# Kernel optimization log

Measured on AMD Instinct MI355X. Metric: run time of the kernel, lower is better.

Reference implementation:

```python
import jax, jax.numpy as jnp
import numpy as np

ENCODER_DIM, DECODER_DIM, ATTN_DIM = 2048, 512, 512
B, P = 128, 196  # batch, num_pixels (14x14)


def setup_inputs() -> dict:
    key = jax.random.key(0)
    ks = jax.random.split(key, 8)
    s_e = 1.0 / np.sqrt(ENCODER_DIM)
    s_d = 1.0 / np.sqrt(DECODER_DIM)
    s_a = 1.0 / np.sqrt(ATTN_DIM)
    return {
        "encoder_out": jax.random.normal(ks[0], (B, P, ENCODER_DIM), jnp.float32),
        "decoder_hidden": jax.random.normal(ks[1], (B, DECODER_DIM), jnp.float32),
        "W_enc": jax.random.uniform(ks[2], (ENCODER_DIM, ATTN_DIM), jnp.float32, -s_e, s_e),
        "b_enc": jax.random.uniform(ks[3], (ATTN_DIM,), jnp.float32, -s_e, s_e),
        "W_dec": jax.random.uniform(ks[4], (DECODER_DIM, ATTN_DIM), jnp.float32, -s_d, s_d),
        "b_dec": jax.random.uniform(ks[5], (ATTN_DIM,), jnp.float32, -s_d, s_d),
        "W_full": jax.random.uniform(ks[6], (ATTN_DIM,), jnp.float32, -s_a, s_a),
        "b_full": jax.random.uniform(ks[7], (), jnp.float32, -s_a, s_a),
    }


def reference(encoder_out, decoder_hidden, W_enc, b_enc, W_dec, b_dec, W_full, b_full):
    # att1: [B, P, A]; att2: [B, A]
    att1 = jnp.einsum("bpe,ea->bpa", encoder_out, W_enc) + b_enc
    att2 = decoder_hidden @ W_dec + b_dec
    # broadcast add + relu + score projection -> [B, P]
    att = jax.nn.relu(att1 + att2[:, None, :]) @ W_full + b_full
    alpha = jax.nn.softmax(att, axis=1)  # over pixels
    # weighted sum over pixels -> [B, E]
    attention_weighted_encoding = jnp.einsum("bpe,bp->be", encoder_out, alpha)
    return (attention_weighted_encoding, alpha)
```

## Files before the change

kernel.cpp:

```cpp
#include <hip/hip_runtime.h>
#include <hip/hip_bf16.h>

#define ENC_DIM 2048
#define DEC_DIM 512
#define ATT_DIM 512
#define BATCH   128
#define NPIX    196
#define NROWS   (BATCH * NPIX)

typedef short bf16x8 __attribute__((ext_vector_type(8)));
typedef float f32x4  __attribute__((ext_vector_type(4)));
typedef unsigned short u16x8 __attribute__((ext_vector_type(8)));

__device__ __forceinline__ unsigned short f2bf(float f) {
    union { float f; unsigned u; } v; v.f = f;
    unsigned r = v.u + 0x7fffu + ((v.u >> 16) & 1u);
    return (unsigned short)(r >> 16);
}

__global__ void k0_transpose(const float* __restrict__ W_enc,
                             unsigned short* __restrict__ Wt) {
    __shared__ float ts[64][65];
    const int a0 = blockIdx.x * 64;
    const int e0 = blockIdx.y * 64;
    const int tx = threadIdx.x & 15;
    const int ty = threadIdx.x >> 4;
    #pragma unroll
    for (int p = 0; p < 4; ++p) {
        const int e = ty + p * 16;
        const float4 v = *(const float4*)&W_enc[(size_t)(e0 + e) * ATT_DIM + a0 + tx * 4];
        ts[e][tx * 4 + 0] = v.x; ts[e][tx * 4 + 1] = v.y;
        ts[e][tx * 4 + 2] = v.z; ts[e][tx * 4 + 3] = v.w;
    }
    __syncthreads();
    #pragma unroll
    for (int p = 0; p < 4; ++p) {
        const int a = ty + p * 16;
        ushort4 u;
        u.x = f2bf(ts[tx * 4 + 0][a]);
        u.y = f2bf(ts[tx * 4 + 1][a]);
        u.z = f2bf(ts[tx * 4 + 2][a]);
        u.w = f2bf(ts[tx * 4 + 3][a]);
        *(ushort4*)&Wt[(size_t)(a0 + a) * ENC_DIM + e0 + tx * 4] = u;
    }
}

__global__ void k1_att2(const float* __restrict__ dh, const float* __restrict__ W_dec,
                        const float* __restrict__ b_dec, const float* __restrict__ b_enc,
                        const float* __restrict__ b_full,
                        float* __restrict__ att2, float* __restrict__ att) {
    __shared__ float dhs[DEC_DIM];
    const int b = blockIdx.x, t = threadIdx.x;
    dhs[t]       = dh[b * DEC_DIM + t];
    dhs[t + 256] = dh[b * DEC_DIM + t + 256];
    __syncthreads();
    float acc0 = 0.f, acc1 = 0.f;
    for (int d = 0; d < DEC_DIM; ++d) {
        const float h = dhs[d];
        acc0 += h * W_dec[d * ATT_DIM + t];
        acc1 += h * W_dec[d * ATT_DIM + t + 256];
    }
    att2[b * ATT_DIM + t]       = acc0 + b_dec[t]       + b_enc[t];
    att2[b * ATT_DIM + t + 256] = acc1 + b_dec[t + 256] + b_enc[t + 256];
    const int gid = b * 256 + t;
    if (gid < NROWS) att[gid] = b_full[0];
}

__launch_bounds__(256, 4)
__global__ void k2_gemm(const float* __restrict__ enc, const unsigned short* __restrict__ Wt,
                        const float* __restrict__ att2, const float* __restrict__ W_full,
                        float* __restrict__ att) {
    __shared__ __align__(16) unsigned short As[64 * 72];
    __shared__ __align__(16) unsigned short Bs[128 * 72];
    __shared__ float att2s[2][128];
    __shared__ float wfs[128];

    const int t    = threadIdx.x;
    const int n0   = blockIdx.x * 128;
    const int row0 = blockIdx.y * 64;
    const int b0   = row0 / NPIX;
    const int rows_left = (b0 + 1) * NPIX - row0;

    if (t < 128) {
        att2s[0][t] = att2[b0 * ATT_DIM + n0 + t];
        att2s[1][t] = (b0 + 1 < BATCH) ? att2[(b0 + 1) * ATT_DIM + n0 + t] : 0.f;
        wfs[t]      = W_full[n0 + t];
    }

    const int w    = t >> 6;
    const int lane = t & 63;
    const int q    = lane >> 4;
    const int cl   = lane & 15;
    const int wm   = (w >> 1) * 32;
    const int wn   = (w & 1) * 64;

    f32x4 acc[2][4] = {};

    const int ar = t >> 3;
    const int ak = (t & 7) * 8;
    const int bn = t >> 2;
    const int bk = (t & 3) * 16;

    const float*          encA = enc + (size_t)(row0 + ar) * ENC_DIM + ak;
    const unsigned short* WtB  = Wt  + (size_t)(n0 + bn)   * ENC_DIM + bk;

    for (int k0 = 0; k0 < ENC_DIM; k0 += 64) {
        __syncthreads();
        #pragma unroll
        for (int p = 0; p < 2; ++p) {
            const float4 v0 = *(const float4*)(encA + (size_t)p * 32 * ENC_DIM + k0);
            const float4 v1 = *(const float4*)(encA + (size_t)p * 32 * ENC_DIM + k0 + 4);
            u16x8 u;
            u[0] = f2bf(v0.x); u[1] = f2bf(v0.y); u[2] = f2bf(v0.z); u[3] = f2bf(v0.w);
            u[4] = f2bf(v1.x); u[5] = f2bf(v1.y); u[6] = f2bf(v1.z); u[7] = f2bf(v1.w);
            *(u16x8*)&As[(ar + p * 32) * 72 + ak] = u;
        }
        #pragma unroll
        for (int p = 0; p < 2; ++p) {
            const uint4 v0 = *(const uint4*)(WtB + (size_t)p * 64 * ENC_DIM + k0);
            const uint4 v1 = *(const uint4*)(WtB + (size_t)p * 64 * ENC_DIM + k0 + 8);
            *(uint4*)&Bs[(bn + p * 64) * 72 + bk]     = v0;
            *(uint4*)&Bs[(bn + p * 64) * 72 + bk + 8] = v1;
        }
        __syncthreads();

        #pragma unroll
        for (int h = 0; h < 2; ++h) {
            bf16x8 af[2], bfr[4];
            #pragma unroll
            for (int i = 0; i < 2; ++i)
                af[i]  = *(const bf16x8*)&As[(wm + i * 16 + cl) * 72 + h * 32 + q * 8];
            #pragma unroll
            for (int i = 0; i < 4; ++i)
                bfr[i] = *(const bf16x8*)&Bs[(wn + i * 16 + cl) * 72 + h * 32 + q * 8];
            #pragma unroll
            for (int mi = 0; mi < 2; ++mi)
                #pragma unroll
                for (int ni = 0; ni < 4; ++ni)
                    acc[mi][ni] = __builtin_amdgcn_mfma_f32_16x16x32_bf16(
                        af[mi], bfr[ni], acc[mi][ni], 0, 0, 0);
        }
    }

    #pragma unroll
    for (int mi = 0; mi < 2; ++mi) {
        float rs[4];
        #pragma unroll
        for (int i = 0; i < 4; ++i) {
            const int lr  = wm + mi * 16 + q * 4 + i;
            const int sel = (lr >= rows_left) ? 1 : 0;
            float sum = 0.f;
            #pragma unroll
            for (int ni = 0; ni < 4; ++ni) {
                const int j = wn + ni * 16 + cl;
                float v = acc[mi][ni][i] + att2s[sel][j];
                v = fmaxf(v, 0.f);
                sum += v * wfs[j];
            }
            rs[i] = sum;
        }
        #pragma unroll
        for (int o = 1; o < 16; o <<= 1) {
            #pragma unroll
            for (int i = 0; i < 4; ++i) rs[i] += __shfl_xor(rs[i], o);
        }
        if (cl == 0) {
            #pragma unroll
            for (int i = 0; i < 4; ++i) {
                const int r = row0 + wm + mi * 16 + q * 4 + i;
                atomicAdd(&att[r], rs[i]);
            }
        }
    }
}

__global__ void k3_softmax(float* __restrict__ att_alpha) {
    __shared__ float red[4];
    const int b = blockIdx.x, t = threadIdx.x;
    const int w = t >> 6, lane = t & 63;
    const float x = (t < NPIX) ? att_alpha[b * NPIX + t] : -INFINITY;
    float m = x;
    #pragma unroll
    for (int o = 32; o >= 1; o >>= 1) m = fmaxf(m, __shfl_xor(m, o));
    if (lane == 0) red[w] = m;
    __syncthreads();
    m = fmaxf(fmaxf(red[0], red[1]), fmaxf(red[2], red[3]));
    const float e = (t < NPIX) ? __expf(x - m) : 0.f;
    float s = e;
    #pragma unroll
    for (int o = 32; o >= 1; o >>= 1) s += __shfl_xor(s, o);
    __syncthreads();
    if (lane == 0) red[w] = s;
    __syncthreads();
    s = red[0] + red[1] + red[2] + red[3];
    if (t < NPIX) att_alpha[b * NPIX + t] = e / s;
}

__global__ void k4_awe(const float* __restrict__ enc, const float* __restrict__ alpha,
                       float* __restrict__ awe) {
    __shared__ float as[NPIX];
    const int b  = blockIdx.y;
    const int t  = threadIdx.x;
    const int e0 = blockIdx.x * 512 + t * 4;
    as[t] = alpha[b * NPIX + t];
    if (t < NPIX - 128) as[t + 128] = alpha[b * NPIX + t + 128];
    __syncthreads();
    const float* base = enc + (size_t)b * NPIX * ENC_DIM + e0;
    f32x4 a[8] = {};
    for (int p = 0; p < 192; p += 8) {
        #pragma unroll
        for (int j = 0; j < 8; ++j) {
            const f32x4 v = *(const f32x4*)(base + (size_t)(p + j) * ENC_DIM);
            a[j] += as[p + j] * v;
        }
    }
    #pragma unroll
    for (int j = 0; j < 4; ++j) {
        const f32x4 v = *(const f32x4*)(base + (size_t)(192 + j) * ENC_DIM);
        a[j] += as[192 + j] * v;
    }
    const f32x4 r = ((a[0] + a[1]) + (a[2] + a[3])) + ((a[4] + a[5]) + (a[6] + a[7]));
    *(f32x4*)&awe[(size_t)b * ENC_DIM + e0] = r;
}

extern "C" void kernel_launch(void* const* d_in, const int* in_sizes, int n_in,
                              void* d_out, int out_size, void* d_ws, size_t ws_size,
                              hipStream_t stream) {
    const float* enc    = (const float*)d_in[0];
    const float* dh     = (const float*)d_in[1];
    const float* W_enc  = (const float*)d_in[2];
    const float* b_enc  = (const float*)d_in[3];
    const float* W_dec  = (const float*)d_in[4];
    const float* b_dec  = (const float*)d_in[5];
    const float* W_full = (const float*)d_in[6];
    const float* b_full = (const float*)d_in[7];

    float* awe   = (float*)d_out;
    float* alpha = awe + BATCH * ENC_DIM;

    unsigned short* Wt   = (unsigned short*)d_ws;
    float*          att2 = (float*)((char*)d_ws + (size_t)ATT_DIM * ENC_DIM * 2);

    k0_transpose<<<dim3(8, 32),  256, 0, stream>>>(W_enc, Wt);
    k1_att2     <<<128,          256, 0, stream>>>(dh, W_dec, b_dec, b_enc, b_full, att2, alpha);
    k2_gemm     <<<dim3(4, 392), 256, 0, stream>>>(enc, Wt, att2, W_full, alpha);
    k3_softmax  <<<128,          256, 0, stream>>>(alpha);
    k4_awe      <<<dim3(4, 128), 128, 0, stream>>>(enc, alpha, awe);
}
```

Before: 435.5 us.

## Enlarge GEMM tile to 128x128 with direct-to-LDS swizzled weight loads

```diff
diff --git a/kernel.cpp b/kernel.cpp
--- a/kernel.cpp
+++ b/kernel.cpp
@@ -16,6 +16,12 @@
     union { float f; unsigned u; } v; v.f = f;
     unsigned r = v.u + 0x7fffu + ((v.u >> 16) & 1u);
     return (unsigned short)(r >> 16);
+}
+
+__device__ __forceinline__ void gload16(const void* g, void* l) {
+    __builtin_amdgcn_global_load_lds(
+        (const __attribute__((address_space(1))) unsigned int*)g,
+        (__attribute__((address_space(3))) unsigned int*)l, 16, 0, 0);
 }
 
 __global__ void k0_transpose(const float* __restrict__ W_enc,
@@ -66,18 +72,19 @@
     if (gid < NROWS) att[gid] = b_full[0];
 }
 
-__launch_bounds__(256, 4)
+__launch_bounds__(256, 3)
 __global__ void k2_gemm(const float* __restrict__ enc, const unsigned short* __restrict__ Wt,
                         const float* __restrict__ att2, const float* __restrict__ W_full,
                         float* __restrict__ att) {
-    __shared__ __align__(16) unsigned short As[64 * 72];
-    __shared__ __align__(16) unsigned short Bs[128 * 72];
+    __shared__ __align__(16) unsigned short As[128 * 72];
+    __shared__ __align__(16) unsigned short Bs[128 * 64];
     __shared__ float att2s[2][128];
     __shared__ float wfs[128];
 
-    const int t    = threadIdx.x;
-    const int n0   = blockIdx.x * 128;
-    const int row0 = blockIdx.y * 64;
+    const int t = threadIdx.x;
+    const int tile = (blockIdx.x & 7) * 98 + (blockIdx.x >> 3);
+    const int n0   = (tile & 3) * 128;
+    const int row0 = (tile >> 2) * 128;
     const int b0   = row0 / NPIX;
     const int rows_left = (b0 + 1) * NPIX - row0;
 
@@ -91,50 +98,48 @@
     const int lane = t & 63;
     const int q    = lane >> 4;
     const int cl   = lane & 15;
-    const int wm   = (w >> 1) * 32;
+    const int wm   = (w >> 1) * 64;
     const int wn   = (w & 1) * 64;
 
-    f32x4 acc[2][4] = {};
+    f32x4 acc[4][4] = {};
 
     const int ar = t >> 3;
     const int ak = (t & 7) * 8;
-    const int bn = t >> 2;
-    const int bk = (t & 3) * 16;
-
-    const float*          encA = enc + (size_t)(row0 + ar) * ENC_DIM + ak;
-    const unsigned short* WtB  = Wt  + (size_t)(n0 + bn)   * ENC_DIM + bk;
-
-    for (int k0 = 0; k0 < ENC_DIM; k0 += 64) {
+    const float* encA = enc + (size_t)(row0 + ar) * ENC_DIM + ak;
+
+    const int br = lane >> 3;
+    const int bc = ((lane & 7) ^ br) * 8;
+    const unsigned short* WtB = Wt + (size_t)(n0 + w * 32 + br) * ENC_DIM + bc;
+
+    for (int kk = 0; kk < ENC_DIM; kk += 64) {
         __syncthreads();
         #pragma unroll
-        for (int p = 0; p < 2; ++p) {
-            const float4 v0 = *(const float4*)(encA + (size_t)p * 32 * ENC_DIM + k0);
-            const float4 v1 = *(const float4*)(encA + (size_t)p * 32 * ENC_DIM + k0 + 4);
+        for (int i = 0; i < 4; ++i)
+            gload16(WtB + (size_t)i * 8 * ENC_DIM + kk,
+                    &Bs[(w * 32 + i * 8) * 64]);
+        #pragma unroll
+        for (int p = 0; p < 4; ++p) {
+            const float4 v0 = *(const float4*)(encA + (size_t)p * 32 * ENC_DIM + kk);
+            const float4 v1 = *(const float4*)(encA + (size_t)p * 32 * ENC_DIM + kk + 4);
             u16x8 u;
             u[0] = f2bf(v0.x); u[1] = f2bf(v0.y); u[2] = f2bf(v0.z); u[3] = f2bf(v0.w);
             u[4] = f2bf(v1.x); u[5] = f2bf(v1.y); u[6] = f2bf(v1.z); u[7] = f2bf(v1.w);
             *(u16x8*)&As[(ar + p * 32) * 72 + ak] = u;
         }
-        #pragma unroll
-        for (int p = 0; p < 2; ++p) {
-            const uint4 v0 = *(const uint4*)(WtB + (size_t)p * 64 * ENC_DIM + k0);
-            const uint4 v1 = *(const uint4*)(WtB + (size_t)p * 64 * ENC_DIM + k0 + 8);
-            *(uint4*)&Bs[(bn + p * 64) * 72 + bk]     = v0;
-            *(uint4*)&Bs[(bn + p * 64) * 72 + bk + 8] = v1;
-        }
         __syncthreads();
 
         #pragma unroll
         for (int h = 0; h < 2; ++h) {
-            bf16x8 af[2], bfr[4];
-            #pragma unroll
-            for (int i = 0; i < 2; ++i)
+            bf16x8 af[4], bfr[4];
+            #pragma unroll
+            for (int i = 0; i < 4; ++i)
                 af[i]  = *(const bf16x8*)&As[(wm + i * 16 + cl) * 72 + h * 32 + q * 8];
             #pragma unroll
             for (int i = 0; i < 4; ++i)
-                bfr[i] = *(const bf16x8*)&Bs[(wn + i * 16 + cl) * 72 + h * 32 + q * 8];
-            #pragma unroll
-            for (int mi = 0; mi < 2; ++mi)
+                bfr[i] = *(const bf16x8*)&Bs[(wn + i * 16 + cl) * 64
+                                             + (((h * 4 + q) ^ (cl & 7)) * 8)];
+            #pragma unroll
+            for (int mi = 0; mi < 4; ++mi)
                 #pragma unroll
                 for (int ni = 0; ni < 4; ++ni)
                     acc[mi][ni] = __builtin_amdgcn_mfma_f32_16x16x32_bf16(
@@ -143,7 +148,7 @@
     }
 
     #pragma unroll
-    for (int mi = 0; mi < 2; ++mi) {
+    for (int mi = 0; mi < 4; ++mi) {
         float rs[4];
         #pragma unroll
         for (int i = 0; i < 4; ++i) {
@@ -243,7 +248,7 @@
 
     k0_transpose<<<dim3(8, 32),  256, 0, stream>>>(W_enc, Wt);
     k1_att2     <<<128,          256, 0, stream>>>(dh, W_dec, b_dec, b_enc, b_full, att2, alpha);
-    k2_gemm     <<<dim3(4, 392), 256, 0, stream>>>(enc, Wt, att2, W_full, alpha);
+    k2_gemm     <<<784,          256, 0, stream>>>(enc, Wt, att2, W_full, alpha);
     k3_softmax  <<<128,          256, 0, stream>>>(alpha);
     k4_awe      <<<dim3(4, 128), 128, 0, stream>>>(enc, alpha, awe);
 }
```

Result: no change. 436.1 us (+0.1%).
